# Performance work log

Measured on AMD Instinct MI355X. Metric: run time of the kernel, lower is better.

## Reference

```python
import jax, jax.numpy as jnp
import numpy as np

N, E, D, R = 50000, 600000, 128, 500


def setup_inputs() -> dict:
    key = jax.random.key(0)
    ks = jax.random.split(key, 9)
    h = jax.random.normal(ks[0], (N, D), dtype=jnp.float32)
    norm = jax.random.uniform(ks[1], (N, 1), dtype=jnp.float32)
    emb_rel = jax.random.normal(ks[2], (R, D), dtype=jnp.float32)
    scale = 1.0 / np.sqrt(D)  # xavier-ish scale for DxD weights
    weight_neighbor = jax.random.normal(ks[3], (D, D), dtype=jnp.float32) * scale
    loop_weight = jax.random.normal(ks[4], (D, D), dtype=jnp.float32) * scale
    evolve_loop_weight = jax.random.normal(ks[5], (D, D), dtype=jnp.float32) * scale
    src = jax.random.randint(ks[6], (E,), 0, N, dtype=jnp.int32)
    dst = jax.random.randint(ks[7], (E,), 0, N, dtype=jnp.int32)
    etype = jax.random.randint(ks[8], (E,), 0, R, dtype=jnp.int32)
    return {
        "h": h, "norm": norm, "emb_rel": emb_rel,
        "weight_neighbor": weight_neighbor, "loop_weight": loop_weight,
        "evolve_loop_weight": evolve_loop_weight,
        "src": src, "dst": dst, "etype": etype,
    }


def reference(h, norm, emb_rel, weight_neighbor, loop_weight,
              evolve_loop_weight, src, dst, etype):
    # msg_func: gather src node features + relation embeddings, add, dense matmul
    msg = (h[src] + emb_rel[etype]) @ weight_neighbor        # [E, D]
    # update_all(fn.sum): scatter-sum messages into destination nodes
    agg = jax.ops.segment_sum(msg, dst, num_segments=N)       # [N, D]
    # apply_func: scale by per-node norm
    h_agg = agg * norm                                        # [N, D]
    # self-loop: nodes with in-degree > 0 use loop_weight, others evolve_loop_weight
    in_deg = jax.ops.segment_sum(jnp.ones((E,), dtype=jnp.float32), dst,
                                 num_segments=N)              # [N]
    loop_msg = jnp.where((in_deg > 0)[:, None],
                         h @ loop_weight,
                         h @ evolve_loop_weight)              # [N, D]
    node_repr = h_agg + loop_msg
    return jax.nn.relu(node_repr)
```

## Files before the change

kernel.cpp:

```cpp
#include <hip/hip_runtime.h>
#include <hip/hip_bf16.h>


#define DIM 128

typedef __attribute__((ext_vector_type(8))) short bf16x8_t;
typedef __attribute__((ext_vector_type(4))) float f32x4_t;

__device__ inline ushort f2bf(float f) {
    __hip_bfloat16 b = __float2bfloat16(f);
    return *reinterpret_cast<ushort*>(&b);
}
__device__ inline float bf2f(ushort u) {
    unsigned v = ((unsigned)u) << 16;
    return __uint_as_float(v);
}
__device__ inline uint4 cvt8(const float4& a, const float4& b) {
    uint4 o;
    o.x = f2bf(a.x) | ((unsigned)f2bf(a.y) << 16);
    o.y = f2bf(a.z) | ((unsigned)f2bf(a.w) << 16);
    o.z = f2bf(b.x) | ((unsigned)f2bf(b.y) << 16);
    o.w = f2bf(b.z) | ((unsigned)f2bf(b.w) << 16);
    return o;
}

__global__ __launch_bounds__(256) void init_kernel(
    const float4* __restrict__ h4, const float4* __restrict__ emb4,
    const float* __restrict__ Wn, const float* __restrict__ Wl,
    uint4* __restrict__ h8, uint4* __restrict__ emb8,
    ushort* __restrict__ Bpack, int* __restrict__ head,
    int nH8, int nE8, int N)
{
    int i = blockIdx.x * 256 + threadIdx.x;
    if (i < nH8) {
        h8[i] = cvt8(h4[2 * i], h4[2 * i + 1]);
        return;
    }
    int j = i - nH8;
    if (j < nE8) {
        emb8[j] = cvt8(emb4[2 * j], emb4[2 * j + 1]);
        return;
    }
    j -= nE8;
    if (j < 32768) {
        int jj   = j & 7;
        int lane = (j >> 3) & 63;
        int ks   = (j >> 9) & 7;
        int nt   = j >> 12;
        int k = ks * 32 + (lane >> 4) * 8 + jj;
        int n = nt * 16 + (lane & 15);
        float v = (k < DIM) ? Wn[k * DIM + n] : Wl[(k - DIM) * DIM + n];
        Bpack[j] = f2bf(v);
        return;
    }
    j -= 32768;
    if (j < N) head[j] = -1;
}

__global__ __launch_bounds__(256) void build_kernel(
    const int4* __restrict__ src4, const int4* __restrict__ dst4,
    const int4* __restrict__ et4, int* __restrict__ head,
    uint2* __restrict__ list, int E4,
    const int* __restrict__ src, const int* __restrict__ dst,
    const int* __restrict__ etype, int E)
{
    int i = blockIdx.x * 256 + threadIdx.x;
    if (i < E4) {
        int4 s = src4[i], d = dst4[i], t = et4[i];
        int e = 4 * i;
        int old;
        old = atomicExch(head + d.x, e + 0);
        list[e + 0] = make_uint2((unsigned)s.x | ((unsigned)t.x << 17), (unsigned)old);
        old = atomicExch(head + d.y, e + 1);
        list[e + 1] = make_uint2((unsigned)s.y | ((unsigned)t.y << 17), (unsigned)old);
        old = atomicExch(head + d.z, e + 2);
        list[e + 2] = make_uint2((unsigned)s.z | ((unsigned)t.z << 17), (unsigned)old);
        old = atomicExch(head + d.w, e + 3);
        list[e + 3] = make_uint2((unsigned)s.w | ((unsigned)t.w << 17), (unsigned)old);
    }
    if (i == 0)
        for (int e = E4 * 4; e < E; ++e) {
            int old = atomicExch(head + dst[e], e);
            list[e] = make_uint2((unsigned)src[e] | ((unsigned)etype[e] << 17),
                                 (unsigned)old);
        }
}

__device__ inline void addbf8(float* a, uint4 hv, uint4 rv) {
    a[0] += bf2f((ushort)(hv.x & 0xFFFF)) + bf2f((ushort)(rv.x & 0xFFFF));
    a[1] += bf2f((ushort)(hv.x >> 16))    + bf2f((ushort)(rv.x >> 16));
    a[2] += bf2f((ushort)(hv.y & 0xFFFF)) + bf2f((ushort)(rv.y & 0xFFFF));
    a[3] += bf2f((ushort)(hv.y >> 16))    + bf2f((ushort)(rv.y >> 16));
    a[4] += bf2f((ushort)(hv.z & 0xFFFF)) + bf2f((ushort)(rv.z & 0xFFFF));
    a[5] += bf2f((ushort)(hv.z >> 16))    + bf2f((ushort)(rv.z >> 16));
    a[6] += bf2f((ushort)(hv.w & 0xFFFF)) + bf2f((ushort)(rv.w & 0xFFFF));
    a[7] += bf2f((ushort)(hv.w >> 16))    + bf2f((ushort)(rv.w >> 16));
}
__device__ inline void store8(uint4* aggn8, int n, int lane, const float* a, float nm) {
    uint4 o;
    o.x = f2bf(a[0] * nm) | ((unsigned)f2bf(a[1] * nm) << 16);
    o.y = f2bf(a[2] * nm) | ((unsigned)f2bf(a[3] * nm) << 16);
    o.z = f2bf(a[4] * nm) | ((unsigned)f2bf(a[5] * nm) << 16);
    o.w = f2bf(a[6] * nm) | ((unsigned)f2bf(a[7] * nm) << 16);
    aggn8[(size_t)n * 16 + lane] = o;
}

__global__ __launch_bounds__(256) void gather_kernel(
    const uint4* __restrict__ h8,
    const uint4* __restrict__ emb8,
    const float* __restrict__ norm,
    const int* __restrict__ head,
    const uint2* __restrict__ list,
    uint4* __restrict__ aggn8,
    int N)
{
    int g = blockIdx.x * 16 + (threadIdx.x >> 4);
    int lane = threadIdx.x & 15;
    int n0 = 2 * g;
    int n1 = 2 * g + 1;
    if (n0 >= N) return;
    bool has1 = (n1 < N);
    int c0 = head[n0];
    int c1 = has1 ? head[n1] : -1;

    float a0[8] = {0.f, 0.f, 0.f, 0.f, 0.f, 0.f, 0.f, 0.f};
    float a1[8] = {0.f, 0.f, 0.f, 0.f, 0.f, 0.f, 0.f, 0.f};

    while ((c0 >= 0) || (c1 >= 0)) {
        bool d0 = (c0 >= 0), d1 = (c1 >= 0);
        uint2 v0, v1;
        uint4 hv0, rv0, hv1, rv1;
        if (d0) v0 = list[c0];
        if (d1) v1 = list[c1];
        if (d0) {
            hv0 = h8[(size_t)(v0.x & 0x1FFFF) * 16 + lane];
            rv0 = emb8[(size_t)(v0.x >> 17) * 16 + lane];
        }
        if (d1) {
            hv1 = h8[(size_t)(v1.x & 0x1FFFF) * 16 + lane];
            rv1 = emb8[(size_t)(v1.x >> 17) * 16 + lane];
        }
        if (d0) { addbf8(a0, hv0, rv0); c0 = (int)v0.y; }
        if (d1) { addbf8(a1, hv1, rv1); c1 = (int)v1.y; }
    }
    store8(aggn8, n0, lane, a0, norm[n0]);
    if (has1) store8(aggn8, n1, lane, a1, norm[n1]);
}

__global__ __launch_bounds__(256) void mfma_gemm_kernel(
    const ushort* __restrict__ aggn_bf,
    const ushort* __restrict__ h_bf,
    const ushort* __restrict__ Bpack,
    const int* __restrict__ head,
    const float* __restrict__ hf,
    const float* __restrict__ We,
    float* __restrict__ out,
    int nRowTiles, int halfWaves)
{
    int wave = threadIdx.x >> 6;
    int lane = threadIdx.x & 63;
    int wid  = blockIdx.x * 4 + wave;
    int ch   = wid & 1;
    int w    = wid >> 1;
    int m    = lane & 15;
    int quad = lane >> 4;

    bf16x8_t b[4][8];
    #pragma unroll
    for (int nt = 0; nt < 4; ++nt)
        #pragma unroll
        for (int ks = 0; ks < 8; ++ks)
            b[nt][ks] = *(const bf16x8_t*)(Bpack +
                (((size_t)(ch * 4 + nt) * 8 + ks) * 64 + lane) * 8);

    for (int rt = w; rt < nRowTiles; rt += halfWaves) {
        size_t rowOff = (size_t)(rt * 16 + m) * DIM + quad * 8;
        bf16x8_t a[8];
        #pragma unroll
        for (int ks = 0; ks < 4; ++ks) {
            a[ks]     = *(const bf16x8_t*)(aggn_bf + rowOff + ks * 32);
            a[ks + 4] = *(const bf16x8_t*)(h_bf   + rowOff + ks * 32);
        }
        f32x4_t acc[4];
        #pragma unroll
        for (int nt = 0; nt < 4; ++nt)
            #pragma unroll
            for (int r = 0; r < 4; ++r) acc[nt][r] = 0.f;

        #pragma unroll
        for (int ks = 0; ks < 8; ++ks)
            #pragma unroll
            for (int nt = 0; nt < 4; ++nt)
                acc[nt] = __builtin_amdgcn_mfma_f32_16x16x32_bf16(
                    a[ks], b[nt][ks], acc[nt], 0, 0, 0);

        int colBase = ch * 64 + m;
        int rowBase = rt * 16 + quad * 4;
        #pragma unroll
        for (int nt = 0; nt < 4; ++nt)
            #pragma unroll
            for (int r = 0; r < 4; ++r)
                out[(size_t)(rowBase + r) * DIM + colBase + nt * 16] =
                    fmaxf(acc[nt][r], 0.f);

        unsigned long long zmask =
            __ballot(head[rt * 16 + (lane & 15)] < 0) & 0xFFFFull;
        while (zmask) {
            int row = __builtin_ctzll(zmask);
            zmask &= zmask - 1;
            int n = rt * 16 + row;
            int c0 = lane * 2;
            float s0 = 0.f, s1 = 0.f;
            for (int k = 0; k < DIM; ++k) {
                float hv = hf[(size_t)n * DIM + k];
                s0 = fmaf(hv, We[(size_t)k * DIM + c0], s0);
                s1 = fmaf(hv, We[(size_t)k * DIM + c0 + 1], s1);
            }
            out[(size_t)n * DIM + c0]     = fmaxf(s0, 0.f);
            out[(size_t)n * DIM + c0 + 1] = fmaxf(s1, 0.f);
        }
    }
}

extern "C" void kernel_launch(void* const* d_in, const int* in_sizes, int n_in,
                              void* d_out, int out_size, void* d_ws, size_t ws_size,
                              hipStream_t stream)
{
    const float* h    = (const float*)d_in[0];
    const float* norm = (const float*)d_in[1];
    const float* emb  = (const float*)d_in[2];
    const float* Wn   = (const float*)d_in[3];
    const float* Wl   = (const float*)d_in[4];
    const float* We   = (const float*)d_in[5];
    const int* src    = (const int*)d_in[6];
    const int* dst    = (const int*)d_in[7];
    const int* etype  = (const int*)d_in[8];

    const int N = in_sizes[1];
    const int E = in_sizes[6];
    const int R = in_sizes[2] / DIM;

    char* p = (char*)d_ws;
    ushort* h_bf    = (ushort*)p;  p += (size_t)N * DIM * 2;
    ushort* emb_bf  = (ushort*)p;  p += (size_t)R * DIM * 2;
    ushort* Bpack   = (ushort*)p;  p += 2 * DIM * DIM * 2;
    ushort* aggn_bf = (ushort*)p;  p += (size_t)N * DIM * 2;
    uint2*  list    = (uint2*)p;   p += (size_t)E * 8;
    int*    head    = (int*)p;

    const int nH8 = N * DIM / 8;
    const int nE8 = R * DIM / 8;
    const int initTotal = nH8 + nE8 + 32768 + N;

    init_kernel<<<dim3((initTotal + 255) / 256), dim3(256), 0, stream>>>(
        (const float4*)h, (const float4*)emb, Wn, Wl,
        (uint4*)h_bf, (uint4*)emb_bf, Bpack, head, nH8, nE8, N);

    build_kernel<<<dim3((E / 4 + 255) / 256), dim3(256), 0, stream>>>(
        (const int4*)src, (const int4*)dst, (const int4*)etype,
        head, list, E / 4, src, dst, etype, E);

    const int nGroups = (N + 1) / 2;
    gather_kernel<<<dim3((nGroups + 15) / 16), dim3(256), 0, stream>>>(
        (const uint4*)h_bf, (const uint4*)emb_bf, norm, head, list,
        (uint4*)aggn_bf, N);

    const int nRowTiles = (N + 15) / 16;
    mfma_gemm_kernel<<<dim3(512), dim3(256), 0, stream>>>(
        aggn_bf, h_bf, Bpack, head, h, We, (float*)d_out, nRowTiles, 1024);
}
```

Before: 176.4 us.

## Overlap self-loop GEMM half with gather in a fused launch

The h @ loop_weight half of the K=256 MFMA GEMM moves into extra blocks of the gather launch, so it runs alongside the memory-bound edge gather and writes a bf16 partial result P1f. The final kernel then does only the aggn @ Wn half and adds the stored partial before ReLU. This cuts the MFMA work on the critical path and uses idle compute during the gather. The cost is an extra N×128 bf16 write and read, plus an extra bf16 rounding of the partial sum.

```diff
diff --git a/kernel.cpp b/kernel.cpp
--- a/kernel.cpp
+++ b/kernel.cpp
@@ -105,52 +105,92 @@
     aggn8[(size_t)n * 16 + lane] = o;
 }
 
-__global__ __launch_bounds__(256) void gather_kernel(
+__global__ __launch_bounds__(256) void gather_p1_kernel(
     const uint4* __restrict__ h8,
     const uint4* __restrict__ emb8,
     const float* __restrict__ norm,
     const int* __restrict__ head,
     const uint2* __restrict__ list,
     uint4* __restrict__ aggn8,
-    int N)
-{
-    int g = blockIdx.x * 16 + (threadIdx.x >> 4);
-    int lane = threadIdx.x & 15;
-    int n0 = 2 * g;
-    int n1 = 2 * g + 1;
-    if (n0 >= N) return;
-    bool has1 = (n1 < N);
-    int c0 = head[n0];
-    int c1 = has1 ? head[n1] : -1;
-
-    float a0[8] = {0.f, 0.f, 0.f, 0.f, 0.f, 0.f, 0.f, 0.f};
-    float a1[8] = {0.f, 0.f, 0.f, 0.f, 0.f, 0.f, 0.f, 0.f};
-
-    while ((c0 >= 0) || (c1 >= 0)) {
-        bool d0 = (c0 >= 0), d1 = (c1 >= 0);
-        uint2 v0, v1;
-        uint4 hv0, rv0, hv1, rv1;
-        if (d0) v0 = list[c0];
-        if (d1) v1 = list[c1];
-        if (d0) {
-            hv0 = h8[(size_t)(v0.x & 0x1FFFF) * 16 + lane];
-            rv0 = emb8[(size_t)(v0.x >> 17) * 16 + lane];
-        }
-        if (d1) {
-            hv1 = h8[(size_t)(v1.x & 0x1FFFF) * 16 + lane];
-            rv1 = emb8[(size_t)(v1.x >> 17) * 16 + lane];
-        }
-        if (d0) { addbf8(a0, hv0, rv0); c0 = (int)v0.y; }
-        if (d1) { addbf8(a1, hv1, rv1); c1 = (int)v1.y; }
-    }
-    store8(aggn8, n0, lane, a0, norm[n0]);
-    if (has1) store8(aggn8, n1, lane, a1, norm[n1]);
-}
-
-__global__ __launch_bounds__(256) void mfma_gemm_kernel(
-    const ushort* __restrict__ aggn_bf,
     const ushort* __restrict__ h_bf,
     const ushort* __restrict__ Bpack,
+    ushort* __restrict__ P1f,
+    int N, int gatherBlocks, int nRowTiles, int p1Waves)
+{
+    if ((int)blockIdx.x < gatherBlocks) {
+        int g = blockIdx.x * 16 + (threadIdx.x >> 4);
+        int lane = threadIdx.x & 15;
+        int n0 = 2 * g;
+        int n1 = 2 * g + 1;
+        if (n0 >= N) return;
+        bool has1 = (n1 < N);
+        int c0 = head[n0];
+        int c1 = has1 ? head[n1] : -1;
+
+        float a0[8] = {0.f, 0.f, 0.f, 0.f, 0.f, 0.f, 0.f, 0.f};
+        float a1[8] = {0.f, 0.f, 0.f, 0.f, 0.f, 0.f, 0.f, 0.f};
+
+        while ((c0 >= 0) || (c1 >= 0)) {
+            bool d0 = (c0 >= 0), d1 = (c1 >= 0);
+            uint2 v0, v1;
+            uint4 hv0, rv0, hv1, rv1;
+            if (d0) v0 = list[c0];
+            if (d1) v1 = list[c1];
+            if (d0) {
+                hv0 = h8[(size_t)(v0.x & 0x1FFFF) * 16 + lane];
+                rv0 = emb8[(size_t)(v0.x >> 17) * 16 + lane];
+            }
+            if (d1) {
+                hv1 = h8[(size_t)(v1.x & 0x1FFFF) * 16 + lane];
+                rv1 = emb8[(size_t)(v1.x >> 17) * 16 + lane];
+            }
+            if (d0) { addbf8(a0, hv0, rv0); c0 = (int)v0.y; }
+            if (d1) { addbf8(a1, hv1, rv1); c1 = (int)v1.y; }
+        }
+        store8(aggn8, n0, lane, a0, norm[n0]);
+        if (has1) store8(aggn8, n1, lane, a1, norm[n1]);
+        return;
+    }
+
+    int wave = threadIdx.x >> 6;
+    int lane = threadIdx.x & 63;
+    int m    = lane & 15;
+    int quad = lane >> 4;
+    int pw   = ((int)blockIdx.x - gatherBlocks) * 4 + wave;
+
+    for (int rt = pw; rt < nRowTiles; rt += p1Waves) {
+        size_t rowOff = (size_t)(rt * 16 + m) * DIM + quad * 8;
+        bf16x8_t a[4];
+        #pragma unroll
+        for (int ks = 0; ks < 4; ++ks)
+            a[ks] = *(const bf16x8_t*)(h_bf + rowOff + ks * 32);
+
+        uint2 o[8];
+        #pragma unroll
+        for (int nt = 0; nt < 8; ++nt) {
+            f32x4_t acc;
+            acc[0] = 0.f; acc[1] = 0.f; acc[2] = 0.f; acc[3] = 0.f;
+            #pragma unroll
+            for (int ks = 0; ks < 4; ++ks) {
+                bf16x8_t b = *(const bf16x8_t*)(Bpack +
+                    (((size_t)nt * 8 + ks + 4) * 64 + lane) * 8);
+                acc = __builtin_amdgcn_mfma_f32_16x16x32_bf16(a[ks], b, acc, 0, 0, 0);
+            }
+            o[nt].x = (unsigned)f2bf(acc[0]) | ((unsigned)f2bf(acc[1]) << 16);
+            o[nt].y = (unsigned)f2bf(acc[2]) | ((unsigned)f2bf(acc[3]) << 16);
+        }
+        uint4* dst = (uint4*)(P1f + ((size_t)rt * 64 + lane) * 32);
+        dst[0] = make_uint4(o[0].x, o[0].y, o[1].x, o[1].y);
+        dst[1] = make_uint4(o[2].x, o[2].y, o[3].x, o[3].y);
+        dst[2] = make_uint4(o[4].x, o[4].y, o[5].x, o[5].y);
+        dst[3] = make_uint4(o[6].x, o[6].y, o[7].x, o[7].y);
+    }
+}
+
+__global__ __launch_bounds__(256) void p2_kernel(
+    const ushort* __restrict__ aggn_bf,
+    const ushort* __restrict__ Bpack,
+    const ushort* __restrict__ P1f,
     const int* __restrict__ head,
     const float* __restrict__ hf,
     const float* __restrict__ We,
@@ -165,34 +205,51 @@
     int m    = lane & 15;
     int quad = lane >> 4;
 
-    bf16x8_t b[4][8];
+    bf16x8_t b[4][4];
     #pragma unroll
     for (int nt = 0; nt < 4; ++nt)
         #pragma unroll
-        for (int ks = 0; ks < 8; ++ks)
+        for (int ks = 0; ks < 4; ++ks)
             b[nt][ks] = *(const bf16x8_t*)(Bpack +
                 (((size_t)(ch * 4 + nt) * 8 + ks) * 64 + lane) * 8);
 
     for (int rt = w; rt < nRowTiles; rt += halfWaves) {
         size_t rowOff = (size_t)(rt * 16 + m) * DIM + quad * 8;
-        bf16x8_t a[8];
-        #pragma unroll
-        for (int ks = 0; ks < 4; ++ks) {
-            a[ks]     = *(const bf16x8_t*)(aggn_bf + rowOff + ks * 32);
-            a[ks + 4] = *(const bf16x8_t*)(h_bf   + rowOff + ks * 32);
-        }
+        bf16x8_t a[4];
+        #pragma unroll
+        for (int ks = 0; ks < 4; ++ks)
+            a[ks] = *(const bf16x8_t*)(aggn_bf + rowOff + ks * 32);
+
         f32x4_t acc[4];
         #pragma unroll
-        for (int nt = 0; nt < 4; ++nt)
-            #pragma unroll
-            for (int r = 0; r < 4; ++r) acc[nt][r] = 0.f;
-
-        #pragma unroll
-        for (int ks = 0; ks < 8; ++ks)
+        for (int nt = 0; nt < 4; ++nt) {
+            acc[nt][0] = 0.f; acc[nt][1] = 0.f; acc[nt][2] = 0.f; acc[nt][3] = 0.f;
+        }
+        #pragma unroll
+        for (int ks = 0; ks < 4; ++ks)
             #pragma unroll
             for (int nt = 0; nt < 4; ++nt)
                 acc[nt] = __builtin_amdgcn_mfma_f32_16x16x32_bf16(
                     a[ks], b[nt][ks], acc[nt], 0, 0, 0);
+
+        const uint4* pp = (const uint4*)(P1f + ((size_t)rt * 64 + lane) * 32 + ch * 16);
+        uint4 p0 = pp[0], p1 = pp[1];
+        acc[0][0] += bf2f((ushort)(p0.x & 0xFFFF));
+        acc[0][1] += bf2f((ushort)(p0.x >> 16));
+        acc[0][2] += bf2f((ushort)(p0.y & 0xFFFF));
+        acc[0][3] += bf2f((ushort)(p0.y >> 16));
+        acc[1][0] += bf2f((ushort)(p0.z & 0xFFFF));
+        acc[1][1] += bf2f((ushort)(p0.z >> 16));
+        acc[1][2] += bf2f((ushort)(p0.w & 0xFFFF));
+        acc[1][3] += bf2f((ushort)(p0.w >> 16));
+        acc[2][0] += bf2f((ushort)(p1.x & 0xFFFF));
+        acc[2][1] += bf2f((ushort)(p1.x >> 16));
+        acc[2][2] += bf2f((ushort)(p1.y & 0xFFFF));
+        acc[2][3] += bf2f((ushort)(p1.y >> 16));
+        acc[3][0] += bf2f((ushort)(p1.z & 0xFFFF));
+        acc[3][1] += bf2f((ushort)(p1.z >> 16));
+        acc[3][2] += bf2f((ushort)(p1.w & 0xFFFF));
+        acc[3][3] += bf2f((ushort)(p1.w >> 16));
 
         int colBase = ch * 64 + m;
         int rowBase = rt * 16 + quad * 4;
@@ -246,7 +303,8 @@
     ushort* Bpack   = (ushort*)p;  p += 2 * DIM * DIM * 2;
     ushort* aggn_bf = (ushort*)p;  p += (size_t)N * DIM * 2;
     uint2*  list    = (uint2*)p;   p += (size_t)E * 8;
-    int*    head    = (int*)p;
+    int*    head    = (int*)p;     p += ((size_t)N * 4 + 15) & ~(size_t)15;
+    ushort* P1f     = (ushort*)p;
 
     const int nH8 = N * DIM / 8;
     const int nE8 = R * DIM / 8;
@@ -261,11 +319,14 @@
         head, list, E / 4, src, dst, etype, E);
 
     const int nGroups = (N + 1) / 2;
-    gather_kernel<<<dim3((nGroups + 15) / 16), dim3(256), 0, stream>>>(
+    const int gatherBlocks = (nGroups + 15) / 16;
+    const int p1Blocks = 256;
+    const int nRowTiles = (N + 15) / 16;
+    gather_p1_kernel<<<dim3(gatherBlocks + p1Blocks), dim3(256), 0, stream>>>(
         (const uint4*)h_bf, (const uint4*)emb_bf, norm, head, list,
-        (uint4*)aggn_bf, N);
-
-    const int nRowTiles = (N + 15) / 16;
-    mfma_gemm_kernel<<<dim3(512), dim3(256), 0, stream>>>(
-        aggn_bf, h_bf, Bpack, head, h, We, (float*)d_out, nRowTiles, 1024);
-}
+        (uint4*)aggn_bf, h_bf, Bpack, P1f,
+        N, gatherBlocks, nRowTiles, p1Blocks * 4);
+
+    p2_kernel<<<dim3(512), dim3(256), 0, stream>>>(
+        aggn_bf, Bpack, P1f, head, h, We, (float*)d_out, nRowTiles, 1024);
+}
```

New measurement: 235.1 us. 33.3% more time.
